# Optimization experiments

Hardware: AMD Instinct MI355X
Metric: run time of the kernel (lower is better)

The kernel has to match this reference:

```python
import jax, jax.numpy as jnp
import numpy as np

D = 1024
H = 16
HD = D // H
FF = 4 * D
EPS = 1e-5


def _ln(x, g, b):
    mu = jnp.mean(x, axis=-1, keepdims=True)
    var = jnp.mean(jnp.square(x - mu), axis=-1, keepdims=True)
    return (x - mu) * jax.lax.rsqrt(var + EPS) * g + b


def setup_inputs() -> dict:
    key = jax.random.key(0)
    ks = jax.random.split(key, 16)
    s = 0.02
    return {
        "x": jax.random.normal(ks[0], (2, 2048, D), dtype=jnp.float32),
        "g1": jnp.ones((D,), jnp.float32),
        "b1": jnp.zeros((D,), jnp.float32),
        "Wqkv": jax.random.normal(ks[1], (D, 3 * D), jnp.float32) * s,
        "bqkv": jnp.zeros((3 * D,), jnp.float32),
        "Wo": jax.random.normal(ks[2], (D, D), jnp.float32) * s,
        "bo": jnp.zeros((D,), jnp.float32),
        "g2": jnp.ones((D,), jnp.float32),
        "b2": jnp.zeros((D,), jnp.float32),
        "W1": jax.random.normal(ks[3], (D, FF), jnp.float32) * s,
        "b1f": jnp.zeros((FF,), jnp.float32),
        "W2": jax.random.normal(ks[4], (FF, D), jnp.float32) * s,
        "b2f": jnp.zeros((D,), jnp.float32),
    }


def reference(x, g1, b1, Wqkv, bqkv, Wo, bo, g2, b2, W1, b1f, W2, b2f):
    b, t, d = x.shape
    residual = x
    h = _ln(x, g1, b1)
    qkv = (h @ Wqkv + bqkv).reshape(b, t, 3, H, HD)
    q, k, v = [jnp.transpose(qkv[:, :, i], (0, 2, 1, 3)) for i in range(3)]  # (b,h,t,hd)
    scale = 1.0 / np.sqrt(HD).astype(np.float32)
    attn = jnp.einsum("bhqd,bhkd->bhqk", q, k) * scale
    # cache_offset = 0 in offline mode: mask = (j < 0) | (j <= i) -> causal
    i = jnp.arange(t)[:, None]
    j = jnp.arange(t)[None, :]
    mask = j <= i
    attn = jnp.where(mask, attn, -jnp.inf)
    attn = jax.nn.softmax(attn, axis=-1)
    out = jnp.einsum("bhqk,bhkd->bhqd", attn, v)
    out = jnp.transpose(out, (0, 2, 1, 3)).reshape(b, t, d)
    x = residual + out @ Wo + bo
    hh = _ln(x, g2, b2)
    ff = jax.nn.gelu(hh @ W1 + b1f, approximate=False) @ W2 + b2f
    return x + ff
```

## Files before the change

kernel.cpp:

```cpp
#include <hip/hip_runtime.h>
#include <math.h>

#define TD 1024
#define NH 16
#define HDIM 64
#define SEQ 2048
#define NB 2
#define NROWS 4096
#define FFD 4096

#define QSCALE 0.18033688011112042f

typedef unsigned short u16;
typedef __attribute__((ext_vector_type(8))) short bf16x8;
typedef __attribute__((ext_vector_type(4))) float f32x4;

__device__ __forceinline__ u16 f2bf(float f) {
    union { float f; unsigned u; } v; v.f = f;
    return (u16)((v.u + 0x7FFFu + ((v.u >> 16) & 1u)) >> 16);
}

__device__ __forceinline__ void async16(void* lds, const void* g) {
    __builtin_amdgcn_global_load_lds(
        (const __attribute__((address_space(1))) unsigned*)g,
        (__attribute__((address_space(3))) unsigned*)lds, 16, 0, 0);
}

__device__ __forceinline__ float gelu_f(float v) {
    float u = 0.7978845608028654f * (v + 0.044715f * v * v * v);
    float e = __expf(2.f * u);
    float th = 1.f - 2.f * __builtin_amdgcn_rcpf(e + 1.f);
    return 0.5f * v * (1.f + th);
}

__global__ __launch_bounds__(256) void ln_bf16(const float* __restrict__ x,
                                               const float* __restrict__ g,
                                               const float* __restrict__ b,
                                               u16* __restrict__ out)
{
    int row = blockIdx.x;
    const float* xr = x + (size_t)row * TD;
    u16* outr = out + (size_t)row * TD;
    int t = threadIdx.x;
    float v[4];
    float s = 0.f, ss = 0.f;
#pragma unroll
    for (int i = 0; i < 4; i++) {
        v[i] = xr[t + 256 * i];
        s += v[i];
        ss += v[i] * v[i];
    }
#pragma unroll
    for (int o = 32; o > 0; o >>= 1) {
        s  += __shfl_down(s, o);
        ss += __shfl_down(ss, o);
    }
    __shared__ float sm[4], sm2[4];
    int wave = t >> 6, lane = t & 63;
    if (lane == 0) { sm[wave] = s; sm2[wave] = ss; }
    __syncthreads();
    s  = sm[0] + sm[1] + sm[2] + sm[3];
    ss = sm2[0] + sm2[1] + sm2[2] + sm2[3];
    float mu  = s * (1.f / TD);
    float var = ss * (1.f / TD) - mu * mu;
    float rstd = rsqrtf(var + 1e-5f);
#pragma unroll
    for (int i = 0; i < 4; i++) {
        int c = t + 256 * i;
        outr[c] = f2bf((v[i] - mu) * rstd * g[c] + b[c]);
    }
}

__global__ __launch_bounds__(256) void prep_kernel(
    const float* __restrict__ Wqkv, const float* __restrict__ Wo,
    const float* __restrict__ W1,   const float* __restrict__ W2,
    u16* __restrict__ wqkvT, u16* __restrict__ woT,
    u16* __restrict__ w1T,   u16* __restrict__ w2T,
    const float* __restrict__ x, const float* __restrict__ g1,
    const float* __restrict__ b1, u16* __restrict__ hbuf)
{
    int blk = blockIdx.x;
    int t = threadIdx.x;
    if (blk >= 3072) {
        int row = blk - 3072;
        const float* xr = x + (size_t)row * TD;
        u16* outr = hbuf + (size_t)row * TD;
        float v[4];
        float s = 0.f, ss = 0.f;
#pragma unroll
        for (int i = 0; i < 4; i++) {
            v[i] = xr[t + 256 * i];
            s += v[i];
            ss += v[i] * v[i];
        }
#pragma unroll
        for (int o = 32; o > 0; o >>= 1) {
            s  += __shfl_down(s, o);
            ss += __shfl_down(ss, o);
        }
        __shared__ float sm[4], sm2[4];
        int wave = t >> 6, lane = t & 63;
        if (lane == 0) { sm[wave] = s; sm2[wave] = ss; }
        __syncthreads();
        s  = sm[0] + sm[1] + sm[2] + sm[3];
        ss = sm2[0] + sm2[1] + sm2[2] + sm2[3];
        float mu  = s * (1.f / TD);
        float var = ss * (1.f / TD) - mu * mu;
        float rstd = rsqrtf(var + 1e-5f);
#pragma unroll
        for (int i = 0; i < 4; i++) {
            int c = t + 256 * i;
            outr[c] = f2bf((v[i] - mu) * rstd * g1[c] + b1[c]);
        }
        return;
    }
    const float* W; u16* Wt; int K, N, local, nx;
    if (blk < 768)       { W = Wqkv; Wt = wqkvT; K = TD;  N = 3 * TD; local = blk;        nx = 48; }
    else if (blk < 1024) { W = Wo;   Wt = woT;   K = TD;  N = TD;     local = blk - 768;  nx = 16; }
    else if (blk < 2048) { W = W1;   Wt = w1T;   K = TD;  N = FFD;    local = blk - 1024; nx = 64; }
    else                 { W = W2;   Wt = w2T;   K = FFD; N = TD;     local = blk - 2048; nx = 16; }
    int n0 = (local % nx) * 64, k0 = (local / nx) * 64;
    __shared__ u16 tile[64][65];
    int c = t & 63, rq = t >> 6;
#pragma unroll
    for (int i = 0; i < 16; i++) {
        int r = rq * 16 + i;
        tile[r][c] = f2bf(W[(size_t)(k0 + r) * N + n0 + c]);
    }
    __syncthreads();
#pragma unroll
    for (int i = 0; i < 16; i++) {
        int r = rq * 16 + i;
        Wt[(size_t)(n0 + r) * K + k0 + c] = tile[c][r];
    }
}

#define EPI_QKV 0
#define EPI_F32RES 1
#define EPI_GELU 2

template<int EPI, int TN, int BK>
__global__ __launch_bounds__(256) void gemm_mfma(int M, int N, int K,
    const u16* __restrict__ A, const u16* __restrict__ Bt,
    const float* __restrict__ bias, const float* __restrict__ res,
    float* __restrict__ Cf, u16* __restrict__ Cb,
    u16* __restrict__ qb, u16* __restrict__ kb, u16* __restrict__ vb)
{
    constexpr int WN  = TN / 2;
    constexpr int NJ  = WN / 16;
    constexpr int KH  = BK / 32;
    constexpr int CPR = BK / 8;
    constexpr int ACH = (128 * CPR) / 256;
    constexpr int BCH = (TN  * CPR) / 256;
    constexpr int ASZ = 128 * BK * 2;
    constexpr int BSZ = TN  * BK * 2;
    __shared__ __align__(16) char smem[2 * (ASZ + BSZ)];

    int t = threadIdx.x;
    int lane = t & 63, w = t >> 6;
    int wm = w >> 1, wn = w & 1;
    int lr = lane & 15, lq = lane >> 4;
    int gx = gridDim.x;
    int lin = blockIdx.x + gx * blockIdx.y;
    int li = lin >> 3;
    int qy = li / gx;
    int ty = (lin & 7) * (gridDim.y >> 3) + qy;
    int tx = li - qy * gx;
    int m0 = ty * 128, n0 = tx * TN;
    int pg = (lq ^ (lr & (CPR - 1))) * 16;

    const u16* ap[ACH];
    const u16* bp[BCH];
#pragma unroll
    for (int i = 0; i < ACH; i++) {
        int c = t + 256 * i, r = c / CPR, s = c % CPR;
        int g = s ^ (r & (CPR - 1));
        ap[i] = A + (size_t)(m0 + r) * K + g * 8;
    }
#pragma unroll
    for (int i = 0; i < BCH; i++) {
        int c = t + 256 * i, r = c / CPR, s = c % CPR;
        int g = s ^ (r & (CPR - 1));
        bp[i] = Bt + (size_t)(n0 + r) * K + g * 8;
    }

    f32x4 acc[4][NJ];
#pragma unroll
    for (int i = 0; i < 4; i++)
#pragma unroll
        for (int j = 0; j < NJ; j++) acc[i][j] = (f32x4){0.f, 0.f, 0.f, 0.f};

#pragma unroll
    for (int i = 0; i < ACH; i++)
        async16(smem + (t + 256 * i) * 16, ap[i]);
#pragma unroll
    for (int i = 0; i < BCH; i++)
        async16(smem + 2 * ASZ + (t + 256 * i) * 16, bp[i]);

    int nk = K / BK;
    for (int kt = 0; kt < nk; kt++) {
        int cur = kt & 1;
        __syncthreads();
        if (kt + 1 < nk) {
            char* An = smem + (1 - cur) * ASZ;
            char* Bn = smem + 2 * ASZ + (1 - cur) * BSZ;
#pragma unroll
            for (int i = 0; i < ACH; i++) {
                ap[i] += BK;
                async16(An + (t + 256 * i) * 16, ap[i]);
            }
#pragma unroll
            for (int i = 0; i < BCH; i++) {
                bp[i] += BK;
                async16(Bn + (t + 256 * i) * 16, bp[i]);
            }
        }
        const char* Ac = smem + cur * ASZ;
        const char* Bc = smem + 2 * ASZ + cur * BSZ;
#pragma unroll
        for (int h = 0; h < KH; h++) {
            bf16x8 af[4], bfr[NJ];
#pragma unroll
            for (int i = 0; i < 4; i++)
                af[i] = *(const bf16x8*)(Ac + (wm * 64 + i * 16 + lr) * (2 * BK) + (pg ^ (h * 64)));
#pragma unroll
            for (int j = 0; j < NJ; j++)
                bfr[j] = *(const bf16x8*)(Bc + (wn * WN + j * 16 + lr) * (2 * BK) + (pg ^ (h * 64)));
#pragma unroll
            for (int i = 0; i < 4; i++)
#pragma unroll
                for (int j = 0; j < NJ; j++)
                    acc[i][j] = __builtin_amdgcn_mfma_f32_16x16x32_bf16(af[i], bfr[j], acc[i][j], 0, 0, 0);
        }
    }

#pragma unroll
    for (int i = 0; i < 4; i++) {
        int rowb = m0 + wm * 64 + i * 16 + lq * 4;
#pragma unroll
        for (int j = 0; j < NJ; j++) {
            int col = n0 + wn * WN + j * 16 + lr;
            float bs = bias[col];
            float vals[4];
#pragma unroll
            for (int r = 0; r < 4; r++) vals[r] = acc[i][j][r] + bs;
            if (EPI == EPI_F32RES) {
#pragma unroll
                for (int r = 0; r < 4; r++) {
                    int rr = rowb + r;
                    Cf[(size_t)rr * N + col] = vals[r] + res[(size_t)rr * N + col];
                }
            } else if (EPI == EPI_GELU) {
#pragma unroll
                for (int r = 0; r < 4; r++)
                    Cb[(size_t)(rowb + r) * N + col] = f2bf(gelu_f(vals[r]));
            } else {
                int comp = col >> 10, cw = col & 1023;
                int h = cw >> 6, d = cw & 63;
                int bb0 = rowb >> 11, ts = rowb & 2047;
                int bh = bb0 * NH + h;
                if (comp == 0) {
#pragma unroll
                    for (int r = 0; r < 4; r++)
                        qb[((size_t)bh * SEQ + ts + r) * HDIM + d] = f2bf(vals[r] * QSCALE);
                } else if (comp == 1) {
#pragma unroll
                    for (int r = 0; r < 4; r++)
                        kb[((size_t)bh * SEQ + ts + r) * HDIM + d] = f2bf(vals[r]);
                } else {
                    ushort4 pk;
                    pk.x = f2bf(vals[0]); pk.y = f2bf(vals[1]);
                    pk.z = f2bf(vals[2]); pk.w = f2bf(vals[3]);
                    *(ushort4*)&vb[((size_t)bh * HDIM + d) * SEQ + ts] = pk;
                }
            }
        }
    }
}

__global__ __launch_bounds__(256, 4) void attn_mfma(const u16* __restrict__ qb,
                                                    const u16* __restrict__ kb,
                                                    const u16* __restrict__ vb,
                                                    u16* __restrict__ ctx)
{
    __shared__ __align__(16) char smem[40960];
    char* QP = smem;
    int lin = blockIdx.x + 32 * blockIdx.y;
    int xcd = lin & 7, idx = lin >> 3;
    int u = idx & 31, v = idx >> 5;
    int bh = xcd + 8 * v;
    int qt = (v & 1) ? u : 31 - u;
    int bb = bh >> 4, h = bh & 15;
    int t = threadIdx.x, lane = t & 63, w = t >> 6;
    int lr = lane & 15, lq = lane >> 4;
    int sw = (lr & 7) * 16;
    int cA = (lq * 16) ^ sw;
    int cB = (64 | (lq * 16)) ^ sw;
    int c0 = t,        r0 = c0 >> 3, g0 = (c0 & 7) ^ (r0 & 7);
    int c1 = t + 256,  r1 = c1 >> 3, g1 = (c1 & 7) ^ (r1 & 7);
    size_t off0  = (size_t)r0 * 128  + g0 * 16;
    size_t off1  = (size_t)r1 * 128  + g1 * 16;
    size_t voff0 = (size_t)r0 * 4096 + g0 * 16;
    size_t voff1 = (size_t)r1 * 4096 + g1 * 16;

    const char* qg_base = (const char*)qb + (size_t)bh * SEQ * 128;
    const char* kg_base = (const char*)kb + (size_t)bh * SEQ * 128;
    const char* vg_base = (const char*)vb + (size_t)bh * 64 * 4096;

    const char* qg = qg_base + (size_t)qt * 8192;
    async16(QP + c0 * 16, qg + off0);
    async16(QP + c1 * 16, qg + off1);
    async16(smem + 8192 + c0 * 16, kg_base + off0);
    async16(smem + 8192 + c1 * 16, kg_base + off1);
    async16(smem + 24576 + c0 * 16, vg_base + voff0);
    async16(smem + 24576 + c1 * 16, vg_base + voff1);

    float mold = -INFINITY, lsum = 0.f;
    f32x4 o[4];
#pragma unroll
    for (int dj = 0; dj < 4; dj++) o[dj] = (f32x4){0.f, 0.f, 0.f, 0.f};
    bf16x8 bq0, bq1;

    for (int kt = 0; kt <= qt; ++kt) {
        int cur = kt & 1;
        __syncthreads();
        if (kt < qt) {
            const char* kgn = kg_base + (size_t)(kt + 1) * 8192;
            const char* vgn = vg_base + (size_t)(kt + 1) * 128;
            char* Kn = smem + 8192  + (1 - cur) * 8192;
            char* Vn = smem + 24576 + (1 - cur) * 8192;
            async16(Kn + c0 * 16, kgn + off0);
            async16(Kn + c1 * 16, kgn + off1);
            async16(Vn + c0 * 16, vgn + voff0);
            async16(Vn + c1 * 16, vgn + voff1);
        }
        if (kt == 0) {
            const char* qr = QP + (w * 16 + lr) * 128;
            bq0 = *(const bf16x8*)(qr + cA);
            bq1 = *(const bf16x8*)(qr + cB);
        }
        const char* Kc = smem + 8192  + cur * 8192;
        const char* Vc = smem + 24576 + cur * 8192;

        float sv[4][4];
        bool diag = (kt == qt);
        __builtin_amdgcn_s_setprio(1);
#pragma unroll
        for (int j = 0; j < 4; ++j) {
            const char* kr = Kc + (j * 16 + lr) * 128;
            bf16x8 ak0 = *(const bf16x8*)(kr + cA);
            bf16x8 ak1 = *(const bf16x8*)(kr + cB);
            f32x4 z = (f32x4){0.f, 0.f, 0.f, 0.f};
            z = __builtin_amdgcn_mfma_f32_16x16x32_bf16(ak0, bq0, z, 0, 0, 0);
            z = __builtin_amdgcn_mfma_f32_16x16x32_bf16(ak1, bq1, z, 0, 0, 0);
#pragma unroll
            for (int r = 0; r < 4; r++) {
                float xv = z[r];
                if (diag && (j * 16 + lq * 4 + r > w * 16 + lr)) xv = -INFINITY;
                sv[j][r] = xv;
            }
        }
        __builtin_amdgcn_s_setprio(0);
        float mx = sv[0][0];
#pragma unroll
        for (int j = 0; j < 4; j++)
#pragma unroll
            for (int r = 0; r < 4; r++) mx = fmaxf(mx, sv[j][r]);
        mx = fmaxf(mx, __shfl_xor(mx, 16));
        mx = fmaxf(mx, __shfl_xor(mx, 32));
        float mnew = fmaxf(mold, mx);
        float alpha = exp2f(mold - mnew);
        float rs = 0.f;
        unsigned pk[4][2];
#pragma unroll
        for (int j = 0; j < 4; j++)
#pragma unroll
            for (int hh = 0; hh < 2; hh++) {
                float p0 = exp2f(sv[j][2 * hh]     - mnew);
                float p1 = exp2f(sv[j][2 * hh + 1] - mnew);
                rs += p0 + p1;
                union { float f; unsigned u; } a0, a1;
                a0.f = p0; a1.f = p1;
                pk[j][hh] = __builtin_amdgcn_perm(a1.u, a0.u, 0x07060302u);
            }
        rs += __shfl_xor(rs, 16);
        rs += __shfl_xor(rs, 32);
        lsum = lsum * alpha + rs;
        mold = mnew;
#pragma unroll
        for (int dj = 0; dj < 4; dj++)
#pragma unroll
            for (int r = 0; r < 4; r++) o[dj][r] *= alpha;

        {
            char* pw = QP + (w * 16 + lr) * 128 + (lq & 1) * 8;
#pragma unroll
            for (int j = 0; j < 4; j++) {
                int pos = ((j * 2 + (lq >> 1)) * 16) ^ sw;
                uint2 u2; u2.x = pk[j][0]; u2.y = pk[j][1];
                *(uint2*)(pw + pos) = u2;
            }
        }
        asm volatile("s_waitcnt lgkmcnt(0)" ::: "memory");
        const char* pr = QP + (w * 16 + lr) * 128;
        bf16x8 bp0 = *(const bf16x8*)(pr + cA);
        bf16x8 bp1 = *(const bf16x8*)(pr + cB);
        __builtin_amdgcn_s_setprio(1);
#pragma unroll
        for (int dj = 0; dj < 4; ++dj) {
            const char* vr = Vc + (dj * 16 + lr) * 128;
            bf16x8 av0 = *(const bf16x8*)(vr + cA);
            bf16x8 av1 = *(const bf16x8*)(vr + cB);
            o[dj] = __builtin_amdgcn_mfma_f32_16x16x32_bf16(av0, bp0, o[dj], 0, 0, 0);
            o[dj] = __builtin_amdgcn_mfma_f32_16x16x32_bf16(av1, bp1, o[dj], 0, 0, 0);
        }
        __builtin_amdgcn_s_setprio(0);
    }

    float inv = 1.f / lsum;
    int tok = qt * 64 + w * 16 + lr;
    u16* cp = ctx + ((size_t)(bb * SEQ) + tok) * TD + h * HDIM + lq * 4;
#pragma unroll
    for (int dj = 0; dj < 4; dj++) {
        ushort4 s4;
        s4.x = f2bf(o[dj][0] * inv); s4.y = f2bf(o[dj][1] * inv);
        s4.z = f2bf(o[dj][2] * inv); s4.w = f2bf(o[dj][3] * inv);
        *(ushort4*)(cp + dj * 16) = s4;
    }
}

extern "C" void kernel_launch(void* const* d_in, const int* in_sizes, int n_in,
                              void* d_out, int out_size, void* d_ws, size_t ws_size,
                              hipStream_t stream)
{
    const float* x    = (const float*)d_in[0];
    const float* g1   = (const float*)d_in[1];
    const float* b1   = (const float*)d_in[2];
    const float* Wqkv = (const float*)d_in[3];
    const float* bqkv = (const float*)d_in[4];
    const float* Wo   = (const float*)d_in[5];
    const float* bo   = (const float*)d_in[6];
    const float* g2   = (const float*)d_in[7];
    const float* b2   = (const float*)d_in[8];
    const float* W1   = (const float*)d_in[9];
    const float* b1f  = (const float*)d_in[10];
    const float* W2   = (const float*)d_in[11];
    const float* b2f  = (const float*)d_in[12];
    float* out = (float*)d_out;

    char* ws = (char*)d_ws;
    const size_t MB = 1ull << 20;
    u16* wqkvT = (u16*)(ws + 0 * MB);
    u16* woT   = (u16*)(ws + 6 * MB);
    u16* w1T   = (u16*)(ws + 8 * MB);
    u16* w2T   = (u16*)(ws + 16 * MB);
    u16* qbuf  = (u16*)(ws + 24 * MB);
    u16* kbuf  = (u16*)(ws + 32 * MB);
    u16* vbuf  = (u16*)(ws + 40 * MB);
    u16* hbuf  = (u16*)(ws + 48 * MB);
    u16* ctx   = (u16*)(ws + 56 * MB);
    float* x2  = (float*)(ws + 64 * MB);
    u16* ff1   = (u16*)(ws + 80 * MB);

    prep_kernel<<<3072 + NROWS, 256, 0, stream>>>(
        Wqkv, Wo, W1, W2, wqkvT, woT, w1T, w2T, x, g1, b1, hbuf);

    gemm_mfma<EPI_QKV, 128, 64><<<dim3(3 * TD / 128, NROWS / 128), 256, 0, stream>>>(
        NROWS, 3 * TD, TD, hbuf, wqkvT, bqkv, nullptr, nullptr, nullptr, qbuf, kbuf, vbuf);
    attn_mfma<<<dim3(32, NB * NH), 256, 0, stream>>>(qbuf, kbuf, vbuf, ctx);
    gemm_mfma<EPI_F32RES, 64, 64><<<dim3(TD / 64, NROWS / 128), 256, 0, stream>>>(
        NROWS, TD, TD, ctx, woT, bo, x, x2, nullptr, nullptr, nullptr, nullptr);
    ln_bf16<<<NROWS, 256, 0, stream>>>(x2, g2, b2, hbuf);
    gemm_mfma<EPI_GELU, 128, 32><<<dim3(FFD / 128, NROWS / 128), 256, 0, stream>>>(
        NROWS, FFD, TD, hbuf, w1T, b1f, nullptr, nullptr, ff1, nullptr, nullptr, nullptr);
    gemm_mfma<EPI_F32RES, 64, 64><<<dim3(TD / 64, NROWS / 128), 256, 0, stream>>>(
        NROWS, TD, FFD, ff1, w2T, b2f, x2, out, nullptr, nullptr, nullptr, nullptr);
}
```

Before: 323.3 us.

## Add dedicated 256x256-tile 512-thread GEMM for FFN up-projection with GELU

Replaces the generic 128-tile GEMM for the W1+GELU stage with a specialized kernel using 256x256 output tiles, 8 waves, double-buffered async LDS loads with XOR swizzle, and an XCD-aware block remap. Larger tiles raise arithmetic intensity and reduce global traffic per FLOP. The tradeoff is only 256 blocks (one wave on the GPU), heavy register use for 32 accumulators per thread, and 128KB of LDS, which limits occupancy.

```diff
diff --git a/kernel.cpp b/kernel.cpp
--- a/kernel.cpp
+++ b/kernel.cpp
@@ -274,6 +274,121 @@
                     *(ushort4*)&vb[((size_t)bh * HDIM + d) * SEQ + ts] = pk;
                 }
             }
+        }
+    }
+}
+
+__global__ __launch_bounds__(512) void gemm256_gelu(
+    const u16* __restrict__ A, const u16* __restrict__ Bt,
+    const float* __restrict__ bias, u16* __restrict__ Cb)
+{
+    constexpr int BK  = 64;
+    constexpr int ASZ = 256 * BK * 2;
+    constexpr int BSZ = 256 * BK * 2;
+    __shared__ __align__(16) char smem[2 * (ASZ + BSZ)];
+
+    int t = threadIdx.x;
+    int lane = t & 63, w = t >> 6;
+    int wm = w >> 2, wn = w & 3;
+    int lr = lane & 15, lq = lane >> 4;
+    int gx = gridDim.x;
+    int lin = blockIdx.x + gx * blockIdx.y;
+    int li = lin >> 3;
+    int qy = li / gx;
+    int ty = (lin & 7) * (gridDim.y >> 3) + qy;
+    int tx = li - qy * gx;
+    int m0 = ty * 256, n0 = tx * 256;
+    int pg = (lq ^ (lr & 7)) * 16;
+
+    const u16* ap[4];
+    const u16* bp[4];
+#pragma unroll
+    for (int i = 0; i < 4; i++) {
+        int c = t + 512 * i, r = c >> 3, s = c & 7;
+        int g = s ^ (r & 7);
+        ap[i] = A  + (size_t)(m0 + r) * TD + g * 8;
+        bp[i] = Bt + (size_t)(n0 + r) * TD + g * 8;
+    }
+
+    f32x4 acc[8][4];
+#pragma unroll
+    for (int i = 0; i < 8; i++)
+#pragma unroll
+        for (int j = 0; j < 4; j++) acc[i][j] = (f32x4){0.f, 0.f, 0.f, 0.f};
+
+#pragma unroll
+    for (int s = 0; s < 2; s++) {
+        char* Ab = smem + s * ASZ;
+        char* Bb = smem + 2 * ASZ + s * BSZ;
+#pragma unroll
+        for (int i = 0; i < 4; i++) {
+            async16(Ab + (t + 512 * i) * 16, ap[i]);
+            ap[i] += BK;
+        }
+#pragma unroll
+        for (int i = 0; i < 4; i++) {
+            async16(Bb + (t + 512 * i) * 16, bp[i]);
+            bp[i] += BK;
+        }
+    }
+
+    constexpr int nk = TD / BK;
+    for (int kt = 0; kt < nk; kt++) {
+        int cur = kt & 1;
+        if (kt + 1 < nk) asm volatile("s_waitcnt vmcnt(8)" ::: "memory");
+        else             asm volatile("s_waitcnt vmcnt(0)" ::: "memory");
+        __builtin_amdgcn_sched_barrier(0);
+        __builtin_amdgcn_s_barrier();
+        __builtin_amdgcn_sched_barrier(0);
+        const char* Ac = smem + cur * ASZ;
+        const char* Bc = smem + 2 * ASZ + cur * BSZ;
+        __builtin_amdgcn_s_setprio(1);
+#pragma unroll
+        for (int h = 0; h < 2; h++) {
+            bf16x8 af[8], bfr[4];
+#pragma unroll
+            for (int i = 0; i < 8; i++)
+                af[i] = *(const bf16x8*)(Ac + (wm * 128 + i * 16 + lr) * 128 + (pg ^ (h * 64)));
+#pragma unroll
+            for (int j = 0; j < 4; j++)
+                bfr[j] = *(const bf16x8*)(Bc + (wn * 64 + j * 16 + lr) * 128 + (pg ^ (h * 64)));
+#pragma unroll
+            for (int i = 0; i < 8; i++)
+#pragma unroll
+                for (int j = 0; j < 4; j++)
+                    acc[i][j] = __builtin_amdgcn_mfma_f32_16x16x32_bf16(af[i], bfr[j], acc[i][j], 0, 0, 0);
+        }
+        __builtin_amdgcn_s_setprio(0);
+        asm volatile("s_waitcnt lgkmcnt(0)" ::: "memory");
+        __builtin_amdgcn_sched_barrier(0);
+        __builtin_amdgcn_s_barrier();
+        __builtin_amdgcn_sched_barrier(0);
+        if (kt + 2 < nk) {
+            char* An = smem + cur * ASZ;
+            char* Bn = smem + 2 * ASZ + cur * BSZ;
+#pragma unroll
+            for (int i = 0; i < 4; i++) {
+                async16(An + (t + 512 * i) * 16, ap[i]);
+                ap[i] += BK;
+            }
+#pragma unroll
+            for (int i = 0; i < 4; i++) {
+                async16(Bn + (t + 512 * i) * 16, bp[i]);
+                bp[i] += BK;
+            }
+        }
+    }
+
+#pragma unroll
+    for (int i = 0; i < 8; i++) {
+        int rowb = m0 + wm * 128 + i * 16 + lq * 4;
+#pragma unroll
+        for (int j = 0; j < 4; j++) {
+            int col = n0 + wn * 64 + j * 16 + lr;
+            float bs = bias[col];
+#pragma unroll
+            for (int r = 0; r < 4; r++)
+                Cb[(size_t)(rowb + r) * FFD + col] = f2bf(gelu_f(acc[i][j][r] + bs));
         }
     }
 }
@@ -471,8 +586,7 @@
     gemm_mfma<EPI_F32RES, 64, 64><<<dim3(TD / 64, NROWS / 128), 256, 0, stream>>>(
         NROWS, TD, TD, ctx, woT, bo, x, x2, nullptr, nullptr, nullptr, nullptr);
     ln_bf16<<<NROWS, 256, 0, stream>>>(x2, g2, b2, hbuf);
-    gemm_mfma<EPI_GELU, 128, 32><<<dim3(FFD / 128, NROWS / 128), 256, 0, stream>>>(
-        NROWS, FFD, TD, hbuf, w1T, b1f, nullptr, nullptr, ff1, nullptr, nullptr, nullptr);
+    gemm256_gelu<<<dim3(FFD / 256, NROWS / 256), 512, 0, stream>>>(hbuf, w1T, b1f, ff1);
     gemm_mfma<EPI_F32RES, 64, 64><<<dim3(TD / 64, NROWS / 128), 256, 0, stream>>>(
         NROWS, TD, FFD, ff1, w2T, b2f, x2, out, nullptr, nullptr, nullptr, nullptr);
 }
```

Result: no change. 320.2 us (-1.0%).
